# Performance work log

Hardware: AMD Instinct MI355X
Metric: run time of the kernel (lower is better)

The kernel has to match this reference:

```python
import jax, jax.numpy as jnp
import numpy as np

DELTA_BEARING = 30.0
DELTA_HEADING = 30.0
N_HEAD = int(360 / DELTA_HEADING)  # 12
N_BEAR = int(360 / DELTA_BEARING)  # 12
B, P, D = 512, 128, 64
EPS = 1e-5


def setup_inputs() -> dict:
    key = jax.random.key(0)
    ks = jax.random.split(key, 8)
    hidden_state = jax.random.normal(ks[0], (B, P, D), dtype=jnp.float32)
    distance_matrix = jax.random.uniform(ks[1], (B, P, P), dtype=jnp.float32) * 10.0
    bearing_matrix = jax.random.uniform(ks[2], (B, P, P), dtype=jnp.float32) * 360.0
    heading_matrix = jax.random.uniform(ks[3], (B, P, P), dtype=jnp.float32) * 360.0
    sequence_mask = (jax.random.uniform(ks[4], (B, P)) < 0.8).astype(jnp.float32)
    domain = jax.random.normal(ks[5], (N_HEAD, N_BEAR), dtype=jnp.float32) * 2.0 + 5.0
    W = jax.random.normal(ks[6], (D, 2 * D), dtype=jnp.float32) / np.sqrt(2 * D)
    b = jnp.zeros((D,), dtype=jnp.float32)
    return {"hidden_state": hidden_state, "distance_matrix": distance_matrix,
            "bearing_matrix": bearing_matrix, "heading_matrix": heading_matrix,
            "sequence_mask": sequence_mask, "domain": domain, "W": W, "b": b}


def reference(hidden_state, distance_matrix, bearing_matrix, heading_matrix,
              sequence_mask, domain, W, b):
    # discretized relative-pose lookup indices
    idx1 = jnp.clip(jnp.floor(heading_matrix / DELTA_HEADING), 0, N_HEAD - 1).astype(jnp.int32)
    idx2 = jnp.clip(jnp.floor(bearing_matrix / DELTA_BEARING), 0, N_BEAR - 1).astype(jnp.int32)
    # gather from learned domain table, subtract distance, relu  -> [B,P,P]
    w = jax.nn.relu(domain[idx1, idx2] - distance_matrix)
    # zero the diagonal (self-interaction) and invalid pedestrian pairs
    eye = jnp.eye(P, dtype=bool)
    pair_mask = sequence_mask[:, :, None] * sequence_mask[:, None, :]  # [B,P,P]
    w = jnp.where(eye[None, :, :], 0.0, w)
    w = jnp.where(pair_mask != 0, w, 0.0)
    # masked softmax over dim=2: mask = (w != 0)
    mask = (w != 0).astype(w.dtype)
    masked_exps = jnp.exp(w) * mask + EPS
    weights = masked_exps / (masked_exps.sum(axis=2, keepdims=True) + EPS)
    # aggregate neighbor hidden states and fuse
    weighted_hidden = jnp.einsum('bpq,bqd->bpd', weights, hidden_state)
    fused = jnp.concatenate([weighted_hidden, hidden_state], axis=2)  # [B,P,2D]
    out = jnp.tanh(fused @ W.T + b)
    return out
```

## Files before the change

### kernel.cpp

```cpp
#include <hip/hip_runtime.h>
#include <hip/hip_bf16.h>
#include <math.h>

#define NB 512
#define NP 128
#define ND 64
#define EPSF 1e-5f
#define SW 136

typedef __attribute__((ext_vector_type(8))) short short8;
typedef __attribute__((ext_vector_type(4))) float f32x4;

#define GLOADX4(dst, voff, base, immstr)                                   \
    asm volatile("global_load_dwordx4 %0, %1, %2 offset:" immstr           \
                 : "=&v"(dst) : "v"(voff), "s"(base))

__device__ __forceinline__ short f2bf(float x) {
    __hip_bfloat16 h = __float2bfloat16(x);
    return *reinterpret_cast<short*>(&h);
}

__device__ __forceinline__ int bin30(float x) {
    float t = (float)((double)x * (1.0 / 30.0));
    int i = (int)t;
    return i < 0 ? 0 : (i > 11 ? 11 : i);
}

__device__ __forceinline__ float fast_tanh(float x) {
    float e = __expf(2.0f * x);
    return 1.0f - 2.0f * __builtin_amdgcn_rcpf(e + 1.0f);
}

__device__ __align__(16) short g_wbf[ND * 2 * ND];

__global__ __launch_bounds__(256) void prep_w(const float* __restrict__ W) {
    int idx = blockIdx.x * 256 + threadIdx.x;
    float4 v = ((const float4*)W)[idx];
    short4 s4;
    s4.x = f2bf(v.x); s4.y = f2bf(v.y); s4.z = f2bf(v.z); s4.w = f2bf(v.w);
    *(short4*)&g_wbf[idx * 4] = s4;
}

__device__ __forceinline__ short8 calc_e8(
    float4 d0, float4 d1, float4 b0, float4 b1, float4 h0, float4 h1,
    float4 m0, float4 m1, const float* s_dom, float mp, int c0, int p)
{
    float dv[8] = {d0.x, d0.y, d0.z, d0.w, d1.x, d1.y, d1.z, d1.w};
    float bv[8] = {b0.x, b0.y, b0.z, b0.w, b1.x, b1.y, b1.z, b1.w};
    float hv[8] = {h0.x, h0.y, h0.z, h0.w, h1.x, h1.y, h1.z, h1.w};
    float mv[8] = {m0.x, m0.y, m0.z, m0.w, m1.x, m1.y, m1.z, m1.w};
    short8 a;
    #pragma unroll
    for (int j = 0; j < 8; ++j) {
        int i1 = bin30(hv[j]), i2 = bin30(bv[j]);
        float wv = s_dom[i1 * 12 + i2] - dv[j];
        bool on = (wv > 0.0f) && (mp != 0.0f) && (mv[j] != 0.0f) && (c0 + j != p);
        a[j] = f2bf(on ? (__expf(wv) + EPSF) : EPSF);
    }
    return a;
}

__global__ __launch_bounds__(256, 2) void spatial_attn_kernel(
    const float* __restrict__ hidden,
    const float* __restrict__ dist,
    const float* __restrict__ bear,
    const float* __restrict__ head,
    const float* __restrict__ smask,
    const float* __restrict__ domain,
    const float* __restrict__ bias,
    float* __restrict__ out)
{
    __shared__ __align__(16) short s_w[64 * SW];
    __shared__ __align__(16) short s_hT[ND * SW];
    __shared__ __align__(16) float s_dom[144];
    __shared__ __align__(16) float s_mask[NP];

    const int blk  = blockIdx.x;
    const int b    = blk >> 1;
    const int half = blk & 1;
    const int tid  = threadIdx.x;
    const int lane = tid & 63;
    const int wave = tid >> 6;
    const int quad = lane >> 4;
    const int l16  = lane & 15;

    const int R0L = wave * 16;
    const int row = R0L + l16;
    const int p   = half * 64 + row;
    const int c0  = quad * 8;

    if (tid < 144) s_dom[tid] = domain[tid];
    if (tid < NP)  s_mask[tid] = smask[b * NP + tid];
    asm volatile("" ::: "memory");

    const unsigned off_m = ((unsigned)(b * NP * NP) + (unsigned)p * NP
                            + (unsigned)c0) * 4u;
    const unsigned perm  = (unsigned)((tid & 15) * 16 + (tid >> 4));
    unsigned offh[8];
    #pragma unroll
    for (int i = 0; i < 8; ++i)
        offh[i] = (unsigned)b * 32768u + (unsigned)(i * 256) * 16u + perm * 16u;

    float4 hv[8];
    GLOADX4(hv[0], offh[0], hidden, "0");
    GLOADX4(hv[1], offh[1], hidden, "0");
    GLOADX4(hv[2], offh[2], hidden, "0");
    GLOADX4(hv[3], offh[3], hidden, "0");
    GLOADX4(hv[4], offh[4], hidden, "0");
    GLOADX4(hv[5], offh[5], hidden, "0");
    GLOADX4(hv[6], offh[6], hidden, "0");
    GLOADX4(hv[7], offh[7], hidden, "0");
    float4 La[12];
    GLOADX4(La[0],  off_m, dist, "0");
    GLOADX4(La[1],  off_m, dist, "16");
    GLOADX4(La[2],  off_m, bear, "0");
    GLOADX4(La[3],  off_m, bear, "16");
    GLOADX4(La[4],  off_m, head, "0");
    GLOADX4(La[5],  off_m, head, "16");
    GLOADX4(La[6],  off_m, dist, "128");
    GLOADX4(La[7],  off_m, dist, "144");
    GLOADX4(La[8],  off_m, bear, "128");
    GLOADX4(La[9],  off_m, bear, "144");
    GLOADX4(La[10], off_m, head, "128");
    GLOADX4(La[11], off_m, head, "144");
    __builtin_amdgcn_sched_barrier(0);

    asm volatile("s_waitcnt vmcnt(12)" ::: "memory");
    __builtin_amdgcn_sched_barrier(0);

    #pragma unroll
    for (int i = 0; i < 8; ++i) {
        int idx = i * 256 + (int)perm;
        int q = idx >> 4;
        int d = (idx & 15) * 4;
        short4 s4;
        s4.x = f2bf(hv[i].x); s4.y = f2bf(hv[i].y);
        s4.z = f2bf(hv[i].z); s4.w = f2bf(hv[i].w);
        s_hT[(d + 0) * SW + q] = s4.x;
        s_hT[(d + 1) * SW + q] = s4.y;
        s_hT[(d + 2) * SW + q] = s4.z;
        s_hT[(d + 3) * SW + q] = s4.w;
        int qloc = q - half * 64;
        if (qloc >= 0 && qloc < 64)
            *(short4*)&s_w[qloc * SW + 64 + d] = s4;
    }
    __syncthreads();

    float4 Lb[12];
    GLOADX4(Lb[0],  off_m, dist, "256");
    GLOADX4(Lb[1],  off_m, dist, "272");
    GLOADX4(Lb[2],  off_m, bear, "256");
    GLOADX4(Lb[3],  off_m, bear, "272");
    GLOADX4(Lb[4],  off_m, head, "256");
    GLOADX4(Lb[5],  off_m, head, "272");
    GLOADX4(Lb[6],  off_m, dist, "384");
    GLOADX4(Lb[7],  off_m, dist, "400");
    GLOADX4(Lb[8],  off_m, bear, "384");
    GLOADX4(Lb[9],  off_m, bear, "400");
    GLOADX4(Lb[10], off_m, head, "384");
    GLOADX4(Lb[11], off_m, head, "400");
    __builtin_amdgcn_sched_barrier(0);

    asm volatile("s_waitcnt vmcnt(12)" ::: "memory");
    __builtin_amdgcn_sched_barrier(0);

    const float mp = s_mask[p];

    f32x4 acc[4], accs;
    #pragma unroll
    for (int tj = 0; tj < 4; ++tj) acc[tj] = (f32x4){0.f, 0.f, 0.f, 0.f};
    accs = (f32x4){0.f, 0.f, 0.f, 0.f};
    short8 ones;
    #pragma unroll
    for (int i = 0; i < 8; ++i) ones[i] = (short)0x3F80;

    #pragma unroll
    for (int k = 0; k < 2; ++k) {
        const int cc = k * 32 + c0;
        float4 m0 = *(const float4*)&s_mask[cc];
        float4 m1 = *(const float4*)&s_mask[cc + 4];
        short8 afr = calc_e8(La[k*6+0], La[k*6+1], La[k*6+2], La[k*6+3],
                             La[k*6+4], La[k*6+5], m0, m1, s_dom, mp, cc, p);
        accs = __builtin_amdgcn_mfma_f32_16x16x32_bf16(afr, ones, accs, 0, 0, 0);
        #pragma unroll
        for (int tj = 0; tj < 4; ++tj) {
            short8 bf = *(const short8*)&s_hT[(tj * 16 + l16) * SW + cc];
            acc[tj] = __builtin_amdgcn_mfma_f32_16x16x32_bf16(afr, bf, acc[tj], 0, 0, 0);
        }
    }

    asm volatile("s_waitcnt vmcnt(0)" ::: "memory");
    __builtin_amdgcn_sched_barrier(0);
    #pragma unroll
    for (int k = 0; k < 2; ++k) {
        const int cc = (k + 2) * 32 + c0;
        float4 m0 = *(const float4*)&s_mask[cc];
        float4 m1 = *(const float4*)&s_mask[cc + 4];
        short8 afr = calc_e8(Lb[k*6+0], Lb[k*6+1], Lb[k*6+2], Lb[k*6+3],
                             Lb[k*6+4], Lb[k*6+5], m0, m1, s_dom, mp, cc, p);
        accs = __builtin_amdgcn_mfma_f32_16x16x32_bf16(afr, ones, accs, 0, 0, 0);
        #pragma unroll
        for (int tj = 0; tj < 4; ++tj) {
            short8 bf = *(const short8*)&s_hT[(tj * 16 + l16) * SW + cc];
            acc[tj] = __builtin_amdgcn_mfma_f32_16x16x32_bf16(afr, bf, acc[tj], 0, 0, 0);
        }
    }

    float inv[4];
    #pragma unroll
    for (int r = 0; r < 4; ++r) inv[r] = 1.0f / (accs[r] + EPSF);

    #pragma unroll
    for (int tj = 0; tj < 4; ++tj)
        #pragma unroll
        for (int r = 0; r < 4; ++r) {
            int rw = R0L + quad * 4 + r;
            s_w[rw * SW + tj * 16 + l16] = f2bf(acc[tj][r] * inv[r]);
        }

    f32x4 acc2[4];
    #pragma unroll
    for (int tj = 0; tj < 4; ++tj) acc2[tj] = (f32x4){0.f, 0.f, 0.f, 0.f};

    #pragma unroll
    for (int kb = 0; kb < 4; ++kb) {
        const int ko = kb * 32 + c0;
        short8 a = *(const short8*)&s_w[(R0L + l16) * SW + ko];
        #pragma unroll
        for (int tj = 0; tj < 4; ++tj) {
            short8 bf = *(const short8*)&g_wbf[(tj * 16 + l16) * (2 * ND) + ko];
            acc2[tj] = __builtin_amdgcn_mfma_f32_16x16x32_bf16(a, bf, acc2[tj], 0, 0, 0);
        }
    }

    float bvals[4];
    #pragma unroll
    for (int tj = 0; tj < 4; ++tj) bvals[tj] = bias[tj * 16 + l16];

    float* ob = out + ((size_t)b * NP + half * 64) * ND;
    #pragma unroll
    for (int tj = 0; tj < 4; ++tj)
        #pragma unroll
        for (int r = 0; r < 4; ++r) {
            int rw = R0L + quad * 4 + r;
            ob[(size_t)rw * ND + tj * 16 + l16] = fast_tanh(acc2[tj][r] + bvals[tj]);
        }
}

extern "C" void kernel_launch(void* const* d_in, const int* in_sizes, int n_in,
                              void* d_out, int out_size, void* d_ws, size_t ws_size,
                              hipStream_t stream) {
    const float* hidden = (const float*)d_in[0];
    const float* dist   = (const float*)d_in[1];
    const float* bear   = (const float*)d_in[2];
    const float* head   = (const float*)d_in[3];
    const float* smask  = (const float*)d_in[4];
    const float* domain = (const float*)d_in[5];
    const float* W      = (const float*)d_in[6];
    const float* bias   = (const float*)d_in[7];
    float* out = (float*)d_out;

    prep_w<<<dim3(8), dim3(256), 0, stream>>>(W);
    spatial_attn_kernel<<<dim3(NB * 2), dim3(256), 0, stream>>>(
        hidden, dist, bear, head, smask, domain, bias, out);
}
```

Baseline: 155.9 us.

## Split fused kernel into exp-compute pass and attention pass via bf16 workspace

```diff
diff --git a/kernel.cpp b/kernel.cpp
--- a/kernel.cpp
+++ b/kernel.cpp
@@ -39,6 +39,171 @@
     short4 s4;
     s4.x = f2bf(v.x); s4.y = f2bf(v.y); s4.z = f2bf(v.z); s4.w = f2bf(v.w);
     *(short4*)&g_wbf[idx * 4] = s4;
+}
+
+
+__global__ __launch_bounds__(256, 8) void calc_e_kernel(
+    const float* __restrict__ dist,
+    const float* __restrict__ bear,
+    const float* __restrict__ head,
+    const float* __restrict__ smask,
+    const float* __restrict__ domain,
+    short* __restrict__ ews)
+{
+    __shared__ __align__(16) float s_dom[144];
+    __shared__ __align__(16) float s_mask[NP];
+
+    const int blk  = blockIdx.x;
+    const int b    = blk >> 2;
+    const int seg  = blk & 3;
+    const int tid  = threadIdx.x;
+    const int lane = tid & 63;
+    const int wave = tid >> 6;
+
+    if (tid < 144) s_dom[tid] = domain[tid];
+    if (tid < NP)  s_mask[tid] = smask[b * NP + tid];
+    __syncthreads();
+
+    const int rsel = lane >> 5;
+    const int q0   = (lane & 31) * 4;
+    const float4 mqv = *(const float4*)&s_mask[q0];
+    const float mv[4] = {mqv.x, mqv.y, mqv.z, mqv.w};
+    const size_t rowbase = (size_t)b * NP * NP;
+
+    #pragma unroll
+    for (int i = 0; i < 4; ++i) {
+        const int p = seg * 32 + i * 8 + wave * 2 + rsel;
+        const size_t ro = rowbase + (size_t)p * NP + q0;
+        float4 dq = *(const float4*)&dist[ro];
+        float4 bq = *(const float4*)&bear[ro];
+        float4 hq = *(const float4*)&head[ro];
+        const float mp = s_mask[p];
+        float dv[4] = {dq.x, dq.y, dq.z, dq.w};
+        float bv[4] = {bq.x, bq.y, bq.z, bq.w};
+        float hv[4] = {hq.x, hq.y, hq.z, hq.w};
+        short ex[4];
+        #pragma unroll
+        for (int c = 0; c < 4; ++c) {
+            int i1 = bin30(hv[c]), i2 = bin30(bv[c]);
+            float wv = s_dom[i1 * 12 + i2] - dv[c];
+            bool on = (wv > 0.0f) && (mp != 0.0f) && (mv[c] != 0.0f) && (q0 + c != p);
+            ex[c] = f2bf(on ? (__expf(wv) + EPSF) : EPSF);
+        }
+        short4 res; res.x = ex[0]; res.y = ex[1]; res.z = ex[2]; res.w = ex[3];
+        *(short4*)&ews[ro] = res;
+    }
+}
+
+__global__ __launch_bounds__(256, 4) void attn_from_e_kernel(
+    const float* __restrict__ hidden,
+    const short* __restrict__ ews,
+    const float* __restrict__ bias,
+    float* __restrict__ out)
+{
+    __shared__ __align__(16) short s_w[64 * SW];
+    __shared__ __align__(16) short s_hT[ND * SW];
+
+    const int blk  = blockIdx.x;
+    const int b    = blk >> 1;
+    const int half = blk & 1;
+    const int tid  = threadIdx.x;
+    const int lane = tid & 63;
+    const int wave = tid >> 6;
+    const int quad = lane >> 4;
+    const int l16  = lane & 15;
+
+    const int R0L = wave * 16;
+    const int P0  = half * 64 + R0L;
+
+    {
+        const short* esrc = ews + ((size_t)b * NP + half * 64) * NP;
+        #pragma unroll
+        for (int i = 0; i < 4; ++i) {
+            int idx = i * 256 + tid;
+            int r  = idx >> 4;
+            int c8 = idx & 15;
+            *(short8*)&s_w[r * SW + c8 * 8] =
+                *(const short8*)&esrc[r * NP + c8 * 8];
+        }
+    }
+    {
+        const float4* hsrc = (const float4*)(hidden + (size_t)b * NP * ND);
+        #pragma unroll
+        for (int i = 0; i < 8; ++i) {
+            int idx = i * 256 + ((tid & 15) * 16 + (tid >> 4));
+            float4 v = hsrc[idx];
+            int q = idx >> 4;
+            int d = (idx & 15) * 4;
+            s_hT[(d + 0) * SW + q] = f2bf(v.x);
+            s_hT[(d + 1) * SW + q] = f2bf(v.y);
+            s_hT[(d + 2) * SW + q] = f2bf(v.z);
+            s_hT[(d + 3) * SW + q] = f2bf(v.w);
+        }
+    }
+    __syncthreads();
+
+    f32x4 acc[4], accs;
+    #pragma unroll
+    for (int tj = 0; tj < 4; ++tj) acc[tj] = (f32x4){0.f, 0.f, 0.f, 0.f};
+    accs = (f32x4){0.f, 0.f, 0.f, 0.f};
+    short8 ones;
+    #pragma unroll
+    for (int i = 0; i < 8; ++i) ones[i] = (short)0x3F80;
+
+    #pragma unroll
+    for (int kb = 0; kb < 4; ++kb) {
+        const int ko = kb * 32 + quad * 8;
+        short8 a = *(const short8*)&s_w[(R0L + l16) * SW + ko];
+        accs = __builtin_amdgcn_mfma_f32_16x16x32_bf16(a, ones, accs, 0, 0, 0);
+        #pragma unroll
+        for (int tj = 0; tj < 4; ++tj) {
+            short8 bf = *(const short8*)&s_hT[(tj * 16 + l16) * SW + ko];
+            acc[tj] = __builtin_amdgcn_mfma_f32_16x16x32_bf16(a, bf, acc[tj], 0, 0, 0);
+        }
+    }
+
+    float inv[4];
+    #pragma unroll
+    for (int r = 0; r < 4; ++r) inv[r] = 1.0f / (accs[r] + EPSF);
+
+    #pragma unroll
+    for (int tj = 0; tj < 4; ++tj)
+        #pragma unroll
+        for (int r = 0; r < 4; ++r) {
+            int rw = R0L + quad * 4 + r;
+            s_w[rw * SW + tj * 16 + l16] = f2bf(acc[tj][r] * inv[r]);
+        }
+    #pragma unroll 4
+    for (int i = 0; i < 16; ++i)
+        s_w[(R0L + i) * SW + 64 + lane] = s_hT[lane * SW + (P0 + i)];
+
+    f32x4 acc2[4];
+    #pragma unroll
+    for (int tj = 0; tj < 4; ++tj) acc2[tj] = (f32x4){0.f, 0.f, 0.f, 0.f};
+
+    #pragma unroll
+    for (int kb = 0; kb < 4; ++kb) {
+        const int ko = kb * 32 + quad * 8;
+        short8 a = *(const short8*)&s_w[(R0L + l16) * SW + ko];
+        #pragma unroll
+        for (int tj = 0; tj < 4; ++tj) {
+            short8 bf = *(const short8*)&g_wbf[(tj * 16 + l16) * (2 * ND) + ko];
+            acc2[tj] = __builtin_amdgcn_mfma_f32_16x16x32_bf16(a, bf, acc2[tj], 0, 0, 0);
+        }
+    }
+
+    float bvals[4];
+    #pragma unroll
+    for (int tj = 0; tj < 4; ++tj) bvals[tj] = bias[tj * 16 + l16];
+
+    float* ob = out + ((size_t)b * NP + half * 64) * ND;
+    #pragma unroll
+    for (int tj = 0; tj < 4; ++tj)
+        #pragma unroll
+        for (int r = 0; r < 4; ++r) {
+            int rw = R0L + quad * 4 + r;
+            ob[(size_t)rw * ND + tj * 16 + l16] = fast_tanh(acc2[tj][r] + bvals[tj]);
+        }
 }
 
 __device__ __forceinline__ short8 calc_e8(
@@ -61,14 +226,10 @@
 }
 
 __global__ __launch_bounds__(256, 2) void spatial_attn_kernel(
-    const float* __restrict__ hidden,
-    const float* __restrict__ dist,
-    const float* __restrict__ bear,
-    const float* __restrict__ head,
-    const float* __restrict__ smask,
-    const float* __restrict__ domain,
-    const float* __restrict__ bias,
-    float* __restrict__ out)
+    const float* __restrict__ hidden, const float* __restrict__ dist,
+    const float* __restrict__ bear, const float* __restrict__ head,
+    const float* __restrict__ smask, const float* __restrict__ domain,
+    const float* __restrict__ bias, float* __restrict__ out)
 {
     __shared__ __align__(16) short s_w[64 * SW];
     __shared__ __align__(16) short s_hT[ND * SW];
@@ -124,7 +285,6 @@
     GLOADX4(La[10], off_m, head, "128");
     GLOADX4(La[11], off_m, head, "144");
     __builtin_amdgcn_sched_barrier(0);
-
     asm volatile("s_waitcnt vmcnt(12)" ::: "memory");
     __builtin_amdgcn_sched_barrier(0);
 
@@ -160,12 +320,10 @@
     GLOADX4(Lb[10], off_m, head, "384");
     GLOADX4(Lb[11], off_m, head, "400");
     __builtin_amdgcn_sched_barrier(0);
-
     asm volatile("s_waitcnt vmcnt(12)" ::: "memory");
     __builtin_amdgcn_sched_barrier(0);
 
     const float mp = s_mask[p];
-
     f32x4 acc[4], accs;
     #pragma unroll
     for (int tj = 0; tj < 4; ++tj) acc[tj] = (f32x4){0.f, 0.f, 0.f, 0.f};
@@ -188,7 +346,6 @@
             acc[tj] = __builtin_amdgcn_mfma_f32_16x16x32_bf16(afr, bf, acc[tj], 0, 0, 0);
         }
     }
-
     asm volatile("s_waitcnt vmcnt(0)" ::: "memory");
     __builtin_amdgcn_sched_barrier(0);
     #pragma unroll
@@ -221,7 +378,6 @@
     f32x4 acc2[4];
     #pragma unroll
     for (int tj = 0; tj < 4; ++tj) acc2[tj] = (f32x4){0.f, 0.f, 0.f, 0.f};
-
     #pragma unroll
     for (int kb = 0; kb < 4; ++kb) {
         const int ko = kb * 32 + c0;
@@ -232,11 +388,9 @@
             acc2[tj] = __builtin_amdgcn_mfma_f32_16x16x32_bf16(a, bf, acc2[tj], 0, 0, 0);
         }
     }
-
     float bvals[4];
     #pragma unroll
     for (int tj = 0; tj < 4; ++tj) bvals[tj] = bias[tj * 16 + l16];
-
     float* ob = out + ((size_t)b * NP + half * 64) * ND;
     #pragma unroll
     for (int tj = 0; tj < 4; ++tj)
@@ -261,6 +415,16 @@
     float* out = (float*)d_out;
 
     prep_w<<<dim3(8), dim3(256), 0, stream>>>(W);
-    spatial_attn_kernel<<<dim3(NB * 2), dim3(256), 0, stream>>>(
-        hidden, dist, bear, head, smask, domain, bias, out);
-}
+
+    const size_t ews_bytes = (size_t)NB * NP * NP * sizeof(short);
+    if (ws_size >= ews_bytes && d_ws != nullptr) {
+        short* ews = (short*)d_ws;
+        calc_e_kernel<<<dim3(NB * 4), dim3(256), 0, stream>>>(
+            dist, bear, head, smask, domain, ews);
+        attn_from_e_kernel<<<dim3(NB * 2), dim3(256), 0, stream>>>(
+            hidden, ews, bias, out);
+    } else {
+        spatial_attn_kernel<<<dim3(NB * 2), dim3(256), 0, stream>>>(
+            hidden, dist, bear, head, smask, domain, bias, out);
+    }
+}
```

New measurement: 168.6 us. +8.1%, slower.
